# Optimization experiments

Hardware: AMD Instinct MI355X
Metric: run time of the kernel (lower is better)

The kernel has to match this reference:

```python
import jax, jax.numpy as jnp
import numpy as np

NH = 8      # nhead in TransformerEncoderLayer(cin, 8, cin, rate)
EPS = 1e-5  # torch LayerNorm default


def _ln(x, g, b):
    m = jnp.mean(x, -1, keepdims=True)
    v = jnp.mean((x - m) ** 2, -1, keepdims=True)
    return (x - m) / jnp.sqrt(v + EPS) * g + b


def _mha(q_in, kv_in, qkv_w, qkv_b, o_w, o_b):
    # q_in: (S, n, c) seq-first, kv_in: (T, n, c); torch MHA packed in_proj
    S, n, c = q_in.shape
    T = kv_in.shape[0]
    dh = c // NH
    q = q_in @ qkv_w[:c].T + qkv_b[:c]
    k = kv_in @ qkv_w[c:2 * c].T + qkv_b[c:2 * c]
    v = kv_in @ qkv_w[2 * c:].T + qkv_b[2 * c:]
    qh = q.reshape(S, n, NH, dh).transpose(1, 2, 0, 3)  # (n, NH, S, dh)
    kh = k.reshape(T, n, NH, dh).transpose(1, 2, 0, 3)
    vh = v.reshape(T, n, NH, dh).transpose(1, 2, 0, 3)
    attn = jax.nn.softmax(jnp.einsum('bhsd,bhtd->bhst', qh, kh) / np.sqrt(dh).astype(np.float32), -1)
    o = jnp.einsum('bhst,bhtd->bhsd', attn, vh).transpose(2, 0, 1, 3).reshape(S, n, c)
    return o @ o_w.T + o_b


def _enc(x, p):
    # torch post-norm encoder layer, relu activation, dropout off (eval)
    (qkv_w, qkv_b, o_w, o_b, ln1w, ln1b, ln2w, ln2b, f1w, f1b, f2w, f2b) = p
    for i in range(qkv_w.shape[0]):
        x = _ln(x + _mha(x, x, qkv_w[i], qkv_b[i], o_w[i], o_b[i]), ln1w[i], ln1b[i])
        h = jax.nn.relu(x @ f1w[i].T + f1b[i]) @ f2w[i].T + f2b[i]
        x = _ln(x + h, ln2w[i], ln2b[i])
    return x


def _dec(x, mem, p):
    (sqkv_w, sqkv_b, so_w, so_b, cqkv_w, cqkv_b, co_w, co_b,
     ln1w, ln1b, ln2w, ln2b, ln3w, ln3b, f1w, f1b, f2w, f2b) = p
    for i in range(sqkv_w.shape[0]):
        x = _ln(x + _mha(x, x, sqkv_w[i], sqkv_b[i], so_w[i], so_b[i]), ln1w[i], ln1b[i])
        x = _ln(x + _mha(x, mem, cqkv_w[i], cqkv_b[i], co_w[i], co_b[i]), ln2w[i], ln2b[i])
        h = jax.nn.relu(x @ f1w[i].T + f1b[i]) @ f2w[i].T + f2b[i]
        x = _ln(x + h, ln3w[i], ln3b[i])
    return x


def _pe2d(c, h, w):
    # standard 2D sinusoidal PE: half channels encode w, half encode h
    half = c // 2
    div = jnp.exp(jnp.arange(0, half, 2, dtype=jnp.float32) * (-np.log(10000.0) / half))
    ph = jnp.arange(h, dtype=jnp.float32)[:, None] * div
    pw = jnp.arange(w, dtype=jnp.float32)[:, None] * div
    pe_h = jnp.stack([jnp.sin(ph), jnp.cos(ph)], -1).reshape(h, half)
    pe_w = jnp.stack([jnp.sin(pw), jnp.cos(pw)], -1).reshape(w, half)
    return jnp.concatenate([
        jnp.broadcast_to(pe_w[None], (h, w, half)),
        jnp.broadcast_to(pe_h[:, None], (h, w, half)),
    ], -1)  # (h, w, c)


def setup_inputs() -> dict:
    key = jax.random.key(0)
    N, C, H, W, K, L = 8, 512, 32, 32, 4096, 6
    ks = iter(jax.random.split(key, 64))
    p = lambda *s: jax.random.normal(next(ks), s, jnp.float32) * 0.02
    return dict(
        x=jax.random.normal(next(ks), (N, C, H, W), jnp.float32),
        pre_w=p(C, C), pre_b=p(C), post_w=p(C, C), post_b=p(C),
        cb_w=p(C, K),  # codebook.weight: (cin, k)
        e_qkv_w=p(L, 3 * C, C), e_qkv_b=p(L, 3 * C), e_o_w=p(L, C, C), e_o_b=p(L, C),
        e_ln1_w=jnp.ones((L, C)), e_ln1_b=jnp.zeros((L, C)),
        e_ln2_w=jnp.ones((L, C)), e_ln2_b=jnp.zeros((L, C)),
        e_f1_w=p(L, C, C), e_f1_b=p(L, C), e_f2_w=p(L, C, C), e_f2_b=p(L, C),
        d_sqkv_w=p(L, 3 * C, C), d_sqkv_b=p(L, 3 * C), d_so_w=p(L, C, C), d_so_b=p(L, C),
        d_cqkv_w=p(L, 3 * C, C), d_cqkv_b=p(L, 3 * C), d_co_w=p(L, C, C), d_co_b=p(L, C),
        d_ln1_w=jnp.ones((L, C)), d_ln1_b=jnp.zeros((L, C)),
        d_ln2_w=jnp.ones((L, C)), d_ln2_b=jnp.zeros((L, C)),
        d_ln3_w=jnp.ones((L, C)), d_ln3_b=jnp.zeros((L, C)),
        d_f1_w=p(L, C, C), d_f1_b=p(L, C), d_f2_w=p(L, C, C), d_f2_b=p(L, C),
        mask=jax.random.bernoulli(next(ks), 0.5, (H * W, N, 1)),  # mixin=1.0 -> p=0.5
    )


def reference(x, pre_w, pre_b, post_w, post_b, cb_w,
              e_qkv_w, e_qkv_b, e_o_w, e_o_b, e_ln1_w, e_ln1_b, e_ln2_w, e_ln2_b,
              e_f1_w, e_f1_b, e_f2_w, e_f2_b,
              d_sqkv_w, d_sqkv_b, d_so_w, d_so_b, d_cqkv_w, d_cqkv_b, d_co_w, d_co_b,
              d_ln1_w, d_ln1_b, d_ln2_w, d_ln2_b, d_ln3_w, d_ln3_b,
              d_f1_w, d_f1_b, d_f2_w, d_f2_b, mask):
    n, c, h, w = x.shape
    S = h * w
    enc_in = jnp.transpose(x, (2, 3, 0, 1))  # (h, w, n, c)
    posisted = (enc_in + _pe2d(c, h, w)[:, :, None, :]).reshape(S, n, c)
    enc_flat = enc_in.reshape(S, n, c)
    y = _enc(posisted, (e_qkv_w, e_qkv_b, e_o_w, e_o_b, e_ln1_w, e_ln1_b,
                        e_ln2_w, e_ln2_b, e_f1_w, e_f1_b, e_f2_w, e_f2_b))
    pre = y @ pre_w.T + pre_b                        # (S, n, c) preProcess
    high = jnp.transpose(pre, (1, 2, 0)).reshape(n, c, h, w)
    sim = jnp.einsum('snc,ck->snk', pre, cb_w)       # similarity (S, n, K)
    logits = jnp.transpose(sim, (1, 0, 2)).reshape(n, h, w, -1)
    soft = jax.nn.softmax(sim, -1) @ cb_w.T          # codebook(softmax) (S, n, c)
    code = jnp.argmax(sim, -1)                        # (S, n)
    hard = cb_w.T[code]                               # one_hot @ cb_w.T == gather
    quant = jax.lax.stop_gradient(hard - soft) + soft  # straight-through
    softs = jnp.transpose(soft, (1, 2, 0)).reshape(n, c, h, w)
    hards = jnp.transpose(hard, (1, 2, 0)).reshape(n, c, h, w)
    post = quant @ post_w.T + post_b                  # postProcess
    mixed = jnp.where(mask, jax.lax.stop_gradient(enc_flat), post)
    dec = _dec(mixed, post, (d_sqkv_w, d_sqkv_b, d_so_w, d_so_b, d_cqkv_w, d_cqkv_b,
                             d_co_w, d_co_b, d_ln1_w, d_ln1_b, d_ln2_w, d_ln2_b,
                             d_ln3_w, d_ln3_b, d_f1_w, d_f1_b, d_f2_w, d_f2_b))
    quantized = jnp.transpose(dec, (1, 2, 0)).reshape(n, c, h, w)
    codes = jnp.transpose(code, (1, 0)).reshape(n, h, w)
    return (quantized, high, softs, hards, codes, logits)
```

## Files before the change

kernel.cpp:

```cpp
#include <hip/hip_runtime.h>
#include <math.h>

#define S_LEN 1024
#define NB 8
#define CDIM 512
#define KCB 4096
#define DH 64
#define NLAYER 6
#define NTOK (S_LEN*NB)
#define TOKC ((long)NTOK*CDIM)

typedef __attribute__((ext_vector_type(8))) _Float16 f16x8;
typedef __attribute__((ext_vector_type(4))) _Float16 f16x4;
typedef __attribute__((ext_vector_type(2))) _Float16 f16x2;
typedef __attribute__((ext_vector_type(4))) float f32x4;

template<int TM, int SPLIT, int F16IN, bool BIAS, bool RES, bool RELU, bool OREMAP, bool E16>
__global__ __launch_bounds__(256)
void hgemm_k(const void* __restrict__ Av, const void* __restrict__ Wv,
             const float* __restrict__ bias, const float* __restrict__ Rsrc, int ldr,
             float* __restrict__ C, int ldc, int M, int N, int K,
             _Float16* __restrict__ Ch16, _Float16* __restrict__ Cl16,
             const void* __restrict__ Avl, const void* __restrict__ Wvl)
{
  constexpr int MI = TM / 32;
  constexpr int ATPR = 256 / TM;
  constexpr int ACOL = 64 / ATPR;
  constexpr bool AF16 = (F16IN >= 1);
  constexpr bool WF16 = (F16IN == 1 || F16IN == 2);
  __shared__ __align__(16) _Float16 Ah[TM*64];
  __shared__ __align__(16) _Float16 Bh[128*64];
  __shared__ __align__(16) _Float16 Al[SPLIT ? TM*64 : 8];
  __shared__ __align__(16) _Float16 Bl[SPLIT ? 128*64 : 8];
  const int t = threadIdx.x;
  const int m0 = blockIdx.y * TM, n0 = blockIdx.x * 128;

  const int arow = t / ATPR, apart = t % ATPR;
  const int brow = t >> 1, bpart = t & 1;

  const float*    Af  = (const float*)Av;
  const _Float16* Axh = (const _Float16*)Av;
  const _Float16* Axl = (const _Float16*)Avl;
  const float*    Wf  = (const float*)Wv;
  const _Float16* Wxh = (const _Float16*)Wv;
  const _Float16* Wxl = (const _Float16*)Wvl;
  const long aoff = (long)(m0 + arow) * K + apart * ACOL;
  const long boff = (long)(n0 + brow) * K + bpart * 32;

  const int lane = t & 63, wave = t >> 6;
  const int wm = wave >> 1, wn = wave & 1;
  const int lr = lane & 15, lk = lane >> 4;

  f32x4 acc[MI][4];
#pragma unroll
  for (int mi = 0; mi < MI; ++mi)
#pragma unroll
    for (int ni = 0; ni < 4; ++ni)
#pragma unroll
      for (int e = 0; e < 4; ++e) acc[mi][ni][e] = 0.f;

  float4 a4[ACOL/4], b4[8];
  f16x8  a16[ACOL/8], b16[4];
  f16x8  a16l[F16IN==2 ? ACOL/8 : 1], b16l[F16IN==2 ? 4 : 1];
  if (AF16) {
#pragma unroll
    for (int g = 0; g < ACOL/8; ++g) a16[g] = *(const f16x8*)(Axh + aoff + g*8);
    if (F16IN == 2) {
#pragma unroll
      for (int g = 0; g < ACOL/8; ++g) a16l[g] = *(const f16x8*)(Axl + aoff + g*8);
    }
  } else {
#pragma unroll
    for (int j = 0; j < ACOL/4; ++j) a4[j] = *(const float4*)(Af + aoff + j*4);
  }
  if (WF16) {
#pragma unroll
    for (int g = 0; g < 4; ++g) b16[g] = *(const f16x8*)(Wxh + boff + g*8);
    if (F16IN == 2) {
#pragma unroll
      for (int g = 0; g < 4; ++g) b16l[g] = *(const f16x8*)(Wxl + boff + g*8);
    }
  } else {
#pragma unroll
    for (int j = 0; j < 8; ++j) b4[j] = *(const float4*)(Wf + boff + j*4);
  }

  for (int k0 = 0; k0 < K; k0 += 64) {
    __syncthreads();
    if (AF16) {
#pragma unroll
      for (int g = 0; g < ACOL/8; ++g) {
        const int sw = (apart*ACOL*2 + g*16) ^ ((arow & 7) << 4);
        *(f16x8*)((char*)Ah + arow*128 + sw) = a16[g];
        if (F16IN == 2) *(f16x8*)((char*)Al + arow*128 + sw) = a16l[g];
      }
    } else {
      const float* af = (const float*)a4;
#pragma unroll
      for (int g = 0; g < ACOL/8; ++g) {
        f16x8 h, l;
#pragma unroll
        for (int j = 0; j < 8; ++j) {
          float xv = af[g*8+j];
          _Float16 hh = (_Float16)xv;
          h[j] = hh;
          if (SPLIT) l[j] = (_Float16)(xv - (float)hh);
        }
        const int sw = (apart*ACOL*2 + g*16) ^ ((arow & 7) << 4);
        *(f16x8*)((char*)Ah + arow*128 + sw) = h;
        if (SPLIT) *(f16x8*)((char*)Al + arow*128 + sw) = l;
      }
    }
    if (WF16) {
#pragma unroll
      for (int g = 0; g < 4; ++g) {
        const int sw = (bpart*64 + g*16) ^ ((brow & 7) << 4);
        *(f16x8*)((char*)Bh + brow*128 + sw) = b16[g];
        if (F16IN == 2) *(f16x8*)((char*)Bl + brow*128 + sw) = b16l[g];
      }
    } else {
      const float* bf = (const float*)b4;
#pragma unroll
      for (int g = 0; g < 4; ++g) {
        f16x8 h, l;
#pragma unroll
        for (int j = 0; j < 8; ++j) {
          float xv = bf[g*8+j];
          _Float16 hh = (_Float16)xv;
          h[j] = hh;
          if (SPLIT) l[j] = (_Float16)(xv - (float)hh);
        }
        const int sw = (bpart*64 + g*16) ^ ((brow & 7) << 4);
        *(f16x8*)((char*)Bh + brow*128 + sw) = h;
        if (SPLIT) *(f16x8*)((char*)Bl + brow*128 + sw) = l;
      }
    }
    __syncthreads();
    if (k0 + 64 < K) {
      if (AF16) {
#pragma unroll
        for (int g = 0; g < ACOL/8; ++g) a16[g] = *(const f16x8*)(Axh + aoff + k0 + 64 + g*8);
        if (F16IN == 2) {
#pragma unroll
          for (int g = 0; g < ACOL/8; ++g) a16l[g] = *(const f16x8*)(Axl + aoff + k0 + 64 + g*8);
        }
      } else {
#pragma unroll
        for (int j = 0; j < ACOL/4; ++j) a4[j] = *(const float4*)(Af + aoff + k0 + 64 + j*4);
      }
      if (WF16) {
#pragma unroll
        for (int g = 0; g < 4; ++g) b16[g] = *(const f16x8*)(Wxh + boff + k0 + 64 + g*8);
        if (F16IN == 2) {
#pragma unroll
          for (int g = 0; g < 4; ++g) b16l[g] = *(const f16x8*)(Wxl + boff + k0 + 64 + g*8);
        }
      } else {
#pragma unroll
        for (int j = 0; j < 8; ++j) b4[j] = *(const float4*)(Wf + boff + k0 + 64 + j*4);
      }
    }
#pragma unroll
    for (int kk = 0; kk < 2; ++kk) {
      f16x8 afh[MI], bfh[4], afl[MI], bfl[4];
#pragma unroll
      for (int mi = 0; mi < MI; ++mi) {
        const int r = wm*(TM/2) + mi*16 + lr;
        const int bo = (lk*16 + kk*64) ^ ((r & 7) << 4);
        afh[mi] = *(const f16x8*)((const char*)Ah + r*128 + bo);
        if (SPLIT) afl[mi] = *(const f16x8*)((const char*)Al + r*128 + bo);
      }
#pragma unroll
      for (int ni = 0; ni < 4; ++ni) {
        const int r = wn*64 + ni*16 + lr;
        const int bo = (lk*16 + kk*64) ^ ((r & 7) << 4);
        bfh[ni] = *(const f16x8*)((const char*)Bh + r*128 + bo);
        if (SPLIT) bfl[ni] = *(const f16x8*)((const char*)Bl + r*128 + bo);
      }
#pragma unroll
      for (int mi = 0; mi < MI; ++mi)
#pragma unroll
        for (int ni = 0; ni < 4; ++ni) {
          acc[mi][ni] = __builtin_amdgcn_mfma_f32_16x16x32_f16(afh[mi], bfh[ni], acc[mi][ni], 0, 0, 0);
          if (SPLIT) {
            acc[mi][ni] = __builtin_amdgcn_mfma_f32_16x16x32_f16(afh[mi], bfl[ni], acc[mi][ni], 0, 0, 0);
            acc[mi][ni] = __builtin_amdgcn_mfma_f32_16x16x32_f16(afl[mi], bfh[ni], acc[mi][ni], 0, 0, 0);
          }
        }
    }
  }

  float bvv[4];
  if (BIAS) {
#pragma unroll
    for (int ni = 0; ni < 4; ++ni) bvv[ni] = bias[n0 + wn*64 + ni*16 + lr];
  }
#pragma unroll
  for (int mi = 0; mi < MI; ++mi)
#pragma unroll
  for (int i = 0; i < 4; ++i) {
    const int rm = m0 + wm*(TM/2) + mi*16 + lk*4 + i;
    long orow = rm;
    if (OREMAP) orow = (long)(rm & (NB-1)) * S_LEN + (rm >> 3);
#pragma unroll
    for (int ni = 0; ni < 4; ++ni) {
      const int col = n0 + wn*64 + ni*16 + lr;
      float v = acc[mi][ni][i];
      if (BIAS) v += bvv[ni];
      if (RES)  v += Rsrc[(long)rm*ldr + col];
      if (RELU) v = fmaxf(v, 0.f);
      if (E16) {
        _Float16 hv = (_Float16)v;
        Ch16[(long)rm*ldc + col] = hv;
        if (SPLIT) Cl16[(long)rm*ldc + col] = (_Float16)(v - (float)hv);
        if (C != nullptr) C[orow*(long)ldc + col] = v;
      } else {
        C[orow*(long)ldc + col] = v;
      }
    }
  }
}

template<int SPLIT>
__global__ __launch_bounds__(256)
void sattn_k(const _Float16* __restrict__ Qh, const _Float16* __restrict__ Ql, int ldq,
             const _Float16* __restrict__ Kh, const _Float16* __restrict__ Kl, int ldk,
             const _Float16* __restrict__ Vh, const _Float16* __restrict__ Vl, int ldv,
             _Float16* __restrict__ Oh, _Float16* __restrict__ Ol, int ldo)
{
  __shared__ __align__(16) char Kb[8192];
  __shared__ __align__(16) char Vb[8192];
  __shared__ __align__(16) char Klo[SPLIT ? 8192 : 16];
  __shared__ __align__(16) char Vlo[SPLIT ? 8192 : 16];

  const int t = threadIdx.x;
  const int b = blockIdx.x >> 3, hd = blockIdx.x & 7;
  const int s0 = blockIdx.y * 128;
  const int qoff = hd * DH;
  const int wave = t >> 6, lane = t & 63;
  const int lr = lane & 15, lk = lane >> 4;
  const int krow = t >> 2, kqd = t & 3;
  const int vtp = t & 31, vdc = t >> 5;

  f16x8 qa[2][2], qal[2][2];
#pragma unroll
  for (int qb = 0; qb < 2; ++qb)
#pragma unroll
    for (int kk = 0; kk < 2; ++kk) {
      const int q = s0 + wave*32 + qb*16 + lr;
      const long base = ((long)q*NB + b)*ldq + qoff + kk*32 + lk*8;
      f16x8 v = *(const f16x8*)(Qh + base);
#pragma unroll
      for (int e = 0; e < 8; ++e) v[e] = v[e] * (_Float16)0.125f;
      qa[qb][kk] = v;
      if (SPLIT) {
        f16x8 w = *(const f16x8*)(Ql + base);
#pragma unroll
        for (int e = 0; e < 8; ++e) w[e] = w[e] * (_Float16)0.125f;
        qal[qb][kk] = w;
      }
    }

  float m_run[2] = {-INFINITY, -INFINITY};
  float l_run[2] = {0.f, 0.f};
  f32x4 oaccT[4][2];
#pragma unroll
  for (int nd = 0; nd < 4; ++nd)
#pragma unroll
    for (int qb = 0; qb < 2; ++qb)
#pragma unroll
      for (int e = 0; e < 4; ++e) oaccT[nd][qb][e] = 0.f;

  f16x8 kr0, kr1, krl0, krl1, vr0, vr1, vrl0, vrl1;
  {
    const long kb = ((long)krow*NB + b)*ldk + qoff + kqd*16;
    kr0 = *(const f16x8*)(Kh + kb);
    kr1 = *(const f16x8*)(Kh + kb + 8);
    if (SPLIT) { krl0 = *(const f16x8*)(Kl + kb); krl1 = *(const f16x8*)(Kl + kb + 8); }
    const long vb = ((long)(2*vtp)*NB + b)*ldv + qoff + vdc*8;
    vr0 = *(const f16x8*)(Vh + vb);
    vr1 = *(const f16x8*)(Vh + vb + (long)NB*ldv);
    if (SPLIT) { vrl0 = *(const f16x8*)(Vl + vb); vrl1 = *(const f16x8*)(Vl + vb + (long)NB*ldv); }
  }

  for (int t0 = 0; t0 < S_LEN; t0 += 64) {
    __syncthreads();
    {
      const int sw0 = (kqd*32) ^ ((krow & 7) << 4);
      const int sw1 = (kqd*32 + 16) ^ ((krow & 7) << 4);
      *(f16x8*)(Kb + krow*128 + sw0) = kr0;
      *(f16x8*)(Kb + krow*128 + sw1) = kr1;
      if (SPLIT) {
        *(f16x8*)(Klo + krow*128 + sw0) = krl0;
        *(f16x8*)(Klo + krow*128 + sw1) = krl1;
      }
#pragma unroll
      for (int j = 0; j < 8; ++j) {
        const int dd = vdc*8 + j;
        const int off = dd*128 + ((vtp*4) ^ ((dd & 7) << 4));
        f16x2 hv = {vr0[j], vr1[j]};
        *(f16x2*)(Vb + off) = hv;
        if (SPLIT) {
          f16x2 lv = {vrl0[j], vrl1[j]};
          *(f16x2*)(Vlo + off) = lv;
        }
      }
    }
    if (t0 + 64 < S_LEN) {
      const long kb = ((long)(t0 + 64 + krow)*NB + b)*ldk + qoff + kqd*16;
      kr0 = *(const f16x8*)(Kh + kb);
      kr1 = *(const f16x8*)(Kh + kb + 8);
      if (SPLIT) { krl0 = *(const f16x8*)(Kl + kb); krl1 = *(const f16x8*)(Kl + kb + 8); }
      const long vb = ((long)(t0 + 64 + 2*vtp)*NB + b)*ldv + qoff + vdc*8;
      vr0 = *(const f16x8*)(Vh + vb);
      vr1 = *(const f16x8*)(Vh + vb + (long)NB*ldv);
      if (SPLIT) { vrl0 = *(const f16x8*)(Vl + vb); vrl1 = *(const f16x8*)(Vl + vb + (long)NB*ldv); }
    }
    __syncthreads();

    f32x4 st[4][2];
#pragma unroll
    for (int ki = 0; ki < 4; ++ki)
#pragma unroll
      for (int qb = 0; qb < 2; ++qb)
#pragma unroll
        for (int e = 0; e < 4; ++e) st[ki][qb][e] = 0.f;
#pragma unroll
    for (int kk = 0; kk < 2; ++kk) {
      f16x8 kb[4], kbl[4];
#pragma unroll
      for (int ki = 0; ki < 4; ++ki) {
        const int r = ki*16 + lr;
        const int bo = (lk*16 + kk*64) ^ ((r & 7) << 4);
        kb[ki] = *(const f16x8*)(Kb + r*128 + bo);
        if (SPLIT) kbl[ki] = *(const f16x8*)(Klo + r*128 + bo);
      }
#pragma unroll
      for (int ki = 0; ki < 4; ++ki)
#pragma unroll
        for (int qb = 0; qb < 2; ++qb) {
          st[ki][qb] = __builtin_amdgcn_mfma_f32_16x16x32_f16(kb[ki], qa[qb][kk], st[ki][qb], 0, 0, 0);
          if (SPLIT) {
            st[ki][qb] = __builtin_amdgcn_mfma_f32_16x16x32_f16(kb[ki], qal[qb][kk], st[ki][qb], 0, 0, 0);
            st[ki][qb] = __builtin_amdgcn_mfma_f32_16x16x32_f16(kbl[ki], qa[qb][kk], st[ki][qb], 0, 0, 0);
          }
        }
    }

    f16x4 pbh[4][2], pbl[4][2];
#pragma unroll
    for (int qb = 0; qb < 2; ++qb) {
      float rm = st[0][qb][0];
#pragma unroll
      for (int ki = 0; ki < 4; ++ki)
#pragma unroll
        for (int e = 0; e < 4; ++e) rm = fmaxf(rm, st[ki][qb][e]);
      rm = fmaxf(rm, __shfl_xor(rm, 16));
      rm = fmaxf(rm, __shfl_xor(rm, 32));
      const float mnew = fmaxf(m_run[qb], rm);
      const float corr = __expf(m_run[qb] - mnew);
      m_run[qb] = mnew;
      float ls = 0.f;
#pragma unroll
      for (int ki = 0; ki < 4; ++ki) {
        f16x4 ph, pl;
#pragma unroll
        for (int e = 0; e < 4; ++e) {
          float p = __expf(st[ki][qb][e] - mnew);
          ls += p;
          _Float16 h = (_Float16)p;
          ph[e] = h;
          if (SPLIT) pl[e] = (_Float16)(p - (float)h);
        }
        pbh[ki][qb] = ph;
        if (SPLIT) pbl[ki][qb] = pl;
      }
      ls += __shfl_xor(ls, 16);
      ls += __shfl_xor(ls, 32);
      l_run[qb] = l_run[qb]*corr + ls;
#pragma unroll
      for (int nd = 0; nd < 4; ++nd)
#pragma unroll
        for (int e = 0; e < 4; ++e) oaccT[nd][qb][e] *= corr;
    }

#pragma unroll
    for (int ki = 0; ki < 4; ++ki) {
      f16x4 avh[4], avl[4];
#pragma unroll
      for (int nd = 0; nd < 4; ++nd) {
        const int row = nd*16 + lr;
        const int bo = (ki*32 + lk*8) ^ ((row & 7) << 4);
        avh[nd] = *(const f16x4*)(Vb + row*128 + bo);
        if (SPLIT) avl[nd] = *(const f16x4*)(Vlo + row*128 + bo);
      }
#pragma unroll
      for (int nd = 0; nd < 4; ++nd)
#pragma unroll
        for (int qb = 0; qb < 2; ++qb) {
          oaccT[nd][qb] = __builtin_amdgcn_mfma_f32_16x16x16f16(avh[nd], pbh[ki][qb], oaccT[nd][qb], 0, 0, 0);
          if (SPLIT) {
            oaccT[nd][qb] = __builtin_amdgcn_mfma_f32_16x16x16f16(avh[nd], pbl[ki][qb], oaccT[nd][qb], 0, 0, 0);
            oaccT[nd][qb] = __builtin_amdgcn_mfma_f32_16x16x16f16(avl[nd], pbh[ki][qb], oaccT[nd][qb], 0, 0, 0);
          }
        }
    }
  }

#pragma unroll
  for (int qb = 0; qb < 2; ++qb) {
    const float inv = 1.0f / l_run[qb];
    const int q = s0 + wave*32 + qb*16 + lr;
    const long base = ((long)q * NB + b) * ldo + qoff;
#pragma unroll
    for (int nd = 0; nd < 4; ++nd) {
      f16x4 o, ol;
#pragma unroll
      for (int e = 0; e < 4; ++e) {
        float v = oaccT[nd][qb][e] * inv;
        _Float16 h = (_Float16)v;
        o[e] = h;
        if (SPLIT) ol[e] = (_Float16)(v - (float)h);
      }
      *(f16x4*)(Oh + base + nd*16 + lk*4) = o;
      if (SPLIT) *(f16x4*)(Ol + base + nd*16 + lk*4) = ol;
    }
  }
}

template<int ES>
__global__ __launch_bounds__(256)
void ln_k(const float* __restrict__ X, const float* __restrict__ g,
          const float* __restrict__ bb, float* __restrict__ Y,
          _Float16* __restrict__ Yh, _Float16* __restrict__ Yl)
{
  const int t = threadIdx.x;
  const int lane = t & 63;
  const long row = (long)blockIdx.x * 4 + (t >> 6);
  const float* xr = X + row * CDIM;
  float4 v0 = *(const float4*)(xr + lane*4);
  float4 v1 = *(const float4*)(xr + 256 + lane*4);
  float s = v0.x+v0.y+v0.z+v0.w + v1.x+v1.y+v1.z+v1.w;
#pragma unroll
  for (int off = 1; off < 64; off <<= 1) s += __shfl_xor(s, off);
  const float mean = s * (1.0f/512.0f);
  float d[8] = {v0.x-mean, v0.y-mean, v0.z-mean, v0.w-mean,
                v1.x-mean, v1.y-mean, v1.z-mean, v1.w-mean};
  float sq = d[0]*d[0]+d[1]*d[1]+d[2]*d[2]+d[3]*d[3]
           + d[4]*d[4]+d[5]*d[5]+d[6]*d[6]+d[7]*d[7];
#pragma unroll
  for (int off = 1; off < 64; off <<= 1) sq += __shfl_xor(sq, off);
  const float inv = 1.0f / sqrtf(sq * (1.0f/512.0f) + 1e-5f);
  float4 g0 = *(const float4*)(g + lane*4);
  float4 g1 = *(const float4*)(g + 256 + lane*4);
  float4 b0 = *(const float4*)(bb + lane*4);
  float4 b1 = *(const float4*)(bb + 256 + lane*4);
  float o[8];
  o[0] = d[0]*inv*g0.x + b0.x; o[1] = d[1]*inv*g0.y + b0.y;
  o[2] = d[2]*inv*g0.z + b0.z; o[3] = d[3]*inv*g0.w + b0.w;
  o[4] = d[4]*inv*g1.x + b1.x; o[5] = d[5]*inv*g1.y + b1.y;
  o[6] = d[6]*inv*g1.z + b1.z; o[7] = d[7]*inv*g1.w + b1.w;
  *(float4*)(Y + row*CDIM + lane*4) = *(float4*)&o[0];
  *(float4*)(Y + row*CDIM + 256 + lane*4) = *(float4*)&o[4];
  if (ES) {
    f16x4 h0, h1, l0, l1;
#pragma unroll
    for (int j = 0; j < 4; ++j) {
      _Float16 h = (_Float16)o[j];     h0[j] = h;
      _Float16 k = (_Float16)o[4+j];   h1[j] = k;
      if (ES == 1) { l0[j] = (_Float16)(o[j] - (float)h); l1[j] = (_Float16)(o[4+j] - (float)k); }
    }
    *(f16x4*)(Yh + row*CDIM + lane*4) = h0;
    *(f16x4*)(Yh + row*CDIM + 256 + lane*4) = h1;
    if (ES == 1) {
      *(f16x4*)(Yl + row*CDIM + lane*4) = l0;
      *(f16x4*)(Yl + row*CDIM + 256 + lane*4) = l1;
    }
  }
}

__global__ void pack_pe_k(const float* __restrict__ x, float* __restrict__ encf,
                          float* __restrict__ posd,
                          _Float16* __restrict__ posh, _Float16* __restrict__ posl)
{
  __shared__ float tl[32][33];
  const int b = blockIdx.z;
  const int s0 = blockIdx.x*32, c0 = blockIdx.y*32;
#pragma unroll
  for (int i = 0; i < 4; ++i) {
    int ci = threadIdx.y + i*8;
    tl[ci][threadIdx.x] = x[((long)b*CDIM + c0+ci)*S_LEN + s0 + threadIdx.x];
  }
  __syncthreads();
#pragma unroll
  for (int i = 0; i < 4; ++i) {
    int si = threadIdx.y + i*8;
    int s = s0 + si;
    int ch = c0 + threadIdx.x;
    float val = tl[threadIdx.x][si];
    long o = ((long)s*NB + b)*CDIM + ch;
    encf[o] = val;
    int pos = (ch < 256) ? (s & 31) : (s >> 5);
    int j = (ch & 255) >> 1;
    float dv = expf((float)(2*j) * (-9.210340371976184f / 256.0f));
    float ang = (float)pos * dv;
    float pe = (ch & 1) ? cosf(ang) : sinf(ang);
    float pv = val + pe;
    posd[o] = pv;
    _Float16 h = (_Float16)pv;
    posh[o] = h;
    posl[o] = (_Float16)(pv - (float)h);
  }
}

__global__ void tpose_k(const float* __restrict__ in, float* __restrict__ out)
{
  __shared__ float tl[32][33];
  const int b = blockIdx.z;
  const int s0 = blockIdx.x*32, c0 = blockIdx.y*32;
#pragma unroll
  for (int i = 0; i < 4; ++i) {
    int si = threadIdx.y + i*8;
    tl[si][threadIdx.x] = in[((long)(s0+si)*NB + b)*CDIM + c0 + threadIdx.x];
  }
  __syncthreads();
#pragma unroll
  for (int i = 0; i < 4; ++i) {
    int ci = threadIdx.y + i*8;
    out[((long)b*CDIM + c0+ci)*S_LEN + s0 + threadIdx.x] = tl[threadIdx.x][ci];
  }
}

__global__ void cbt16_k(const float* __restrict__ cb,
                        _Float16* __restrict__ outh, _Float16* __restrict__ outl)
{
  __shared__ float tl[32][33];
  const int k0 = blockIdx.x*32, c0 = blockIdx.y*32;
#pragma unroll
  for (int i = 0; i < 4; ++i) {
    int ci = threadIdx.y + i*8;
    tl[ci][threadIdx.x] = cb[(long)(c0+ci)*KCB + k0 + threadIdx.x];
  }
  __syncthreads();
#pragma unroll
  for (int i = 0; i < 4; ++i) {
    int ki = threadIdx.y + i*8;
    float v = tl[threadIdx.x][ki];
    _Float16 h = (_Float16)v;
    outh[(long)(k0+ki)*CDIM + c0 + threadIdx.x] = h;
    outl[(long)(k0+ki)*CDIM + c0 + threadIdx.x] = (_Float16)(v - (float)h);
  }
}

__global__ __launch_bounds__(256)
void conv16_k(const float* __restrict__ in, _Float16* __restrict__ out)
{
  const long i = ((long)blockIdx.x * 256 + threadIdx.x) * 8;
  float4 v0 = *(const float4*)(in + i);
  float4 v1 = *(const float4*)(in + i + 4);
  f16x8 h;
  h[0]=(_Float16)v0.x; h[1]=(_Float16)v0.y; h[2]=(_Float16)v0.z; h[3]=(_Float16)v0.w;
  h[4]=(_Float16)v1.x; h[5]=(_Float16)v1.y; h[6]=(_Float16)v1.z; h[7]=(_Float16)v1.w;
  *(f16x8*)(out + i) = h;
}

__global__ __launch_bounds__(256)
void convsplit_k(const float* __restrict__ in, _Float16* __restrict__ oh,
                 _Float16* __restrict__ ol)
{
  const long i = ((long)blockIdx.x * 256 + threadIdx.x) * 8;
  float4 v0 = *(const float4*)(in + i);
  float4 v1 = *(const float4*)(in + i + 4);
  float vv[8] = {v0.x,v0.y,v0.z,v0.w,v1.x,v1.y,v1.z,v1.w};
  f16x8 h, l;
#pragma unroll
  for (int j = 0; j < 8; ++j) {
    _Float16 hh = (_Float16)vv[j];
    h[j] = hh;
    l[j] = (_Float16)(vv[j] - (float)hh);
  }
  *(f16x8*)(oh + i) = h;
  *(f16x8*)(ol + i) = l;
}

__global__ __launch_bounds__(256)
void simstats_k(const float* __restrict__ logits, _Float16* __restrict__ Pbuf,
                int* __restrict__ codes_tok, float* __restrict__ codes_out)
{
  const long phys = blockIdx.x;
  const float* rowp = logits + phys * KCB;
  const int t = threadIdx.x;
  float vals[16];
#pragma unroll
  for (int rep = 0; rep < 4; ++rep) {
    float4 v = *(const float4*)(rowp + rep*1024 + t*4);
    vals[rep*4+0]=v.x; vals[rep*4+1]=v.y; vals[rep*4+2]=v.z; vals[rep*4+3]=v.w;
  }
  float mv = -INFINITY; int mi = 0;
#pragma unroll
  for (int rep = 0; rep < 4; ++rep)
#pragma unroll
    for (int j = 0; j < 4; ++j) {
      float xv = vals[rep*4+j];
      int ix = rep*1024 + t*4 + j;
      if (xv > mv) { mv = xv; mi = ix; }
    }
  const int lane = t & 63, wid = t >> 6;
#pragma unroll
  for (int off = 1; off < 64; off <<= 1) {
    float ov = __shfl_xor(mv, off);
    int   oi = __shfl_xor(mi, off);
    if (ov > mv || (ov == mv && oi < mi)) { mv = ov; mi = oi; }
  }
  __shared__ float smax[4]; __shared__ int sidx[4]; __shared__ float ssum[4];
  __shared__ float fm; __shared__ int fi; __shared__ float sinv;
  if (lane == 0) { smax[wid] = mv; sidx[wid] = mi; }
  __syncthreads();
  if (t == 0) {
    float bm = smax[0]; int bi = sidx[0];
    for (int wq = 1; wq < 4; ++wq)
      if (smax[wq] > bm || (smax[wq] == bm && sidx[wq] < bi)) { bm = smax[wq]; bi = sidx[wq]; }
    fm = bm; fi = bi;
  }
  __syncthreads();
  const float Mx = fm;
  float se = 0.f;
#pragma unroll
  for (int q = 0; q < 16; ++q) se += __expf(vals[q] - Mx);
#pragma unroll
  for (int off = 1; off < 64; off <<= 1) se += __shfl_xor(se, off);
  if (lane == 0) ssum[wid] = se;
  __syncthreads();
  const int b = (int)(phys >> 10), s = (int)(phys & 1023);
  if (t == 0) {
    float tot = ssum[0]+ssum[1]+ssum[2]+ssum[3];
    sinv = 1.0f / tot;
    codes_tok[s*NB + b] = fi;
    codes_out[phys] = (float)fi;
  }
  __syncthreads();
  const float inv = sinv;
  _Float16* prow = Pbuf + ((long)s*NB + b) * KCB;
#pragma unroll
  for (int rep = 0; rep < 4; ++rep) {
    f16x4 pv;
#pragma unroll
    for (int j = 0; j < 4; ++j) pv[j] = (_Float16)(__expf(vals[rep*4+j] - Mx) * inv);
    *(f16x4*)(prow + rep*1024 + t*4) = pv;
  }
}

__global__ __launch_bounds__(128)
void quant_k(const float* __restrict__ soft, const int* __restrict__ codes_tok,
             const _Float16* __restrict__ cbh, const _Float16* __restrict__ cbl,
             float* __restrict__ quant, float* __restrict__ hardb,
             _Float16* __restrict__ qh16)
{
  const int r = blockIdx.x;
  const int code = codes_tok[r];
  const int c = threadIdx.x * 4;
  f16x4 hh = *(const f16x4*)(cbh + (long)code*CDIM + c);
  f16x4 hl = *(const f16x4*)(cbl + (long)code*CDIM + c);
  float4 sf = *(const float4*)(soft + (long)r*CDIM + c);
  float4 h, q;
  h.x = (float)hh[0] + (float)hl[0]; h.y = (float)hh[1] + (float)hl[1];
  h.z = (float)hh[2] + (float)hl[2]; h.w = (float)hh[3] + (float)hl[3];
  q.x = (h.x - sf.x) + sf.x; q.y = (h.y - sf.y) + sf.y;
  q.z = (h.z - sf.z) + sf.z; q.w = (h.w - sf.w) + sf.w;
  *(float4*)(quant + (long)r*CDIM + c) = q;
  *(float4*)(hardb + (long)r*CDIM + c) = h;
  f16x4 qh = {(_Float16)q.x, (_Float16)q.y, (_Float16)q.z, (_Float16)q.w};
  *(f16x4*)(qh16 + (long)r*CDIM + c) = qh;
}

__global__ void maskdetect_k(const void* __restrict__ mask, int* __restrict__ flag)
{
  const unsigned int* wds = (const unsigned int*)mask;
  int t = threadIdx.x;
  int okI = 1, okF = 1, okL = 1;
  for (int i = t; i < 2048; i += 256) {
    unsigned int u = wds[i];
    if (u > 1u) okI = 0;
    if (u != 0u && u != 0x3F800000u) okF = 0;
    if ((i & 1) ? (u != 0u) : (u > 1u)) okL = 0;
  }
  __shared__ int sI, sF, sL;
  if (t == 0) { sI = 1; sF = 1; sL = 1; }
  __syncthreads();
  if (!okI) atomicAnd(&sI, 0);
  if (!okF) atomicAnd(&sF, 0);
  if (!okL) atomicAnd(&sL, 0);
  __syncthreads();
  if (t == 0) {
    int f;
    if (sI && sL) f = 3;
    else if (sI)  f = 1;
    else if (sF)  f = 2;
    else          f = 0;
    *flag = f;
  }
}

__global__ __launch_bounds__(256)
void mixed_k(const float* __restrict__ encf, const float* __restrict__ post,
             const void* __restrict__ mask, const int* __restrict__ flag,
             float* __restrict__ outx, _Float16* __restrict__ outh)
{
  long gid = (long)blockIdx.x * blockDim.x + threadIdx.x;
  int r = (int)(gid >> 7);
  int c = (int)(gid & 127) * 4;
  int f = *flag;
  bool mv;
  if (f == 0)      mv = ((const unsigned char*)mask)[r] != 0;
  else if (f == 1) mv = ((const int*)mask)[r] != 0;
  else if (f == 3) mv = ((const long long*)mask)[r] != 0;
  else             mv = ((const float*)mask)[r] != 0.0f;
  const float* src = mv ? encf : post;
  float4 v = *(const float4*)(src + (long)r*CDIM + c);
  *(float4*)(outx + (long)r*CDIM + c) = v;
  f16x4 h = {(_Float16)v.x, (_Float16)v.y, (_Float16)v.z, (_Float16)v.w};
  *(f16x4*)(outh + (long)r*CDIM + c) = h;
}

extern "C" void kernel_launch(void* const* d_in, const int* in_sizes, int n_in,
                              void* d_out, int out_size, void* d_ws, size_t ws_size,
                              hipStream_t stream)
{
  const float* x       = (const float*)d_in[0];
  const float* pre_w   = (const float*)d_in[1];
  const float* pre_b   = (const float*)d_in[2];
  const float* post_w  = (const float*)d_in[3];
  const float* post_b  = (const float*)d_in[4];
  const float* cb_w    = (const float*)d_in[5];
  const float* e_qkv_w = (const float*)d_in[6];
  const float* e_qkv_b = (const float*)d_in[7];
  const float* e_o_w   = (const float*)d_in[8];
  const float* e_o_b   = (const float*)d_in[9];
  const float* e_ln1_w = (const float*)d_in[10];
  const float* e_ln1_b = (const float*)d_in[11];
  const float* e_ln2_w = (const float*)d_in[12];
  const float* e_ln2_b = (const float*)d_in[13];
  const float* e_f1_w  = (const float*)d_in[14];
  const float* e_f1_b  = (const float*)d_in[15];
  const float* e_f2_w  = (const float*)d_in[16];
  const float* e_f2_b  = (const float*)d_in[17];
  const float* d_sqkv_w= (const float*)d_in[18];
  const float* d_sqkv_b= (const float*)d_in[19];
  const float* d_so_w  = (const float*)d_in[20];
  const float* d_so_b  = (const float*)d_in[21];
  const float* d_cqkv_w= (const float*)d_in[22];
  const float* d_cqkv_b= (const float*)d_in[23];
  const float* d_co_w  = (const float*)d_in[24];
  const float* d_co_b  = (const float*)d_in[25];
  const float* d_ln1w  = (const float*)d_in[26];
  const float* d_ln1b  = (const float*)d_in[27];
  const float* d_ln2w  = (const float*)d_in[28];
  const float* d_ln2b  = (const float*)d_in[29];
  const float* d_ln3w  = (const float*)d_in[30];
  const float* d_ln3b  = (const float*)d_in[31];
  const float* d_f1w   = (const float*)d_in[32];
  const float* d_f1b   = (const float*)d_in[33];
  const float* d_f2w   = (const float*)d_in[34];
  const float* d_f2b   = (const float*)d_in[35];
  const void*  mask    = d_in[36];

  float* out = (float*)d_out;
  float* o_quant  = out;
  float* o_high   = out + 4194304;
  float* o_softs  = out + 8388608;
  float* o_hards  = out + 12582912;
  float* o_codes  = out + 16777216;
  float* o_logits = out + 16785408;

  float* ws    = (float*)d_ws;
  float* ENC   = ws;
  float* Xb    = ws + TOKC;
  float* T1    = ws + 2*TOKC;
  float* T2    = ws + 3*TOKC;
  float* QKV   = ws + 4*TOKC;
  float* MEMB  = ws + 7*TOKC;
  float* CBREG = ws + 8*TOKC;
  int*   CODES = (int*)(CBREG + (long)KCB*CDIM);
  int*   FLAG  = CODES + NTOK;
  float* HARDB = QKV;
  float* QUANT = QKV + TOKC;
  _Float16* PBUF = (_Float16*)QKV;
  _Float16* CBH  = (_Float16*)T1;
  _Float16* QKVh = (_Float16*)QKV;
  _Float16* QKVl = QKVh + (long)NTOK*3*CDIM;
  _Float16* CQh  = (_Float16*)QKV;
  _Float16* KVh  = (_Float16*)(QKV + TOKC);
  _Float16* CBT16h = (_Float16*)CBREG;
  _Float16* CBT16l = CBT16h + (long)KCB*CDIM;
  _Float16* PREH = (_Float16*)T2;
  _Float16* PREL = PREH + TOKC;
  _Float16* AH16   = (_Float16*)ENC;
  _Float16* FH16   = AH16 + TOKC;
  _Float16* XH16   = ((_Float16*)QKV) + 4*TOKC;
  _Float16* MEMBH16= XH16 + TOKC;
  _Float16* QH16   = ((_Float16*)T1) + TOKC;

  const long WQSZ = (long)6*3*CDIM*CDIM;
  const long WSSZ = (long)6*CDIM*CDIM;
  _Float16* SCR  = (_Float16*)o_logits;
  _Float16* WQH = SCR;            _Float16* WQL = WQH + WQSZ;
  _Float16* WOH = WQL + WQSZ;     _Float16* WOL = WOH + WSSZ;
  _Float16* WF1H= WOL + WSSZ;     _Float16* WF1L= WF1H + WSSZ;
  _Float16* WF2H= WF1L + WSSZ;    _Float16* WF2L= WF2H + WSSZ;
  _Float16* WPH = WF2L + WSSZ;    _Float16* WPL = WPH + (long)CDIM*CDIM;
  _Float16* XH  = WPL + (long)CDIM*CDIM;  _Float16* XL  = XH + TOKC;
  _Float16* AH  = XL + TOKC;      _Float16* AL  = AH + TOKC;
  _Float16* L1H = AL + TOKC;      _Float16* L1L = L1H + TOKC;
  _Float16* H1H = L1L + TOKC;     _Float16* H1L = H1H + TOKC;

  _Float16* DWSQ = (_Float16*)MEMB;
  _Float16* DWCQ = (_Float16*)T1;
  _Float16* DWF1 = DWCQ + WQSZ;
  _Float16* DWF2 = DWF1 + WSSZ;
  _Float16* DWSO = (_Float16*)CBREG;
  _Float16* DWCO = DWSO + WSSZ;

  const size_t NEED = (size_t)(8*TOKC + (long)KCB*CDIM + 2*NTOK + NTOK + 16) * 4;
  if (ws_size < NEED) return;

  const int M = NTOK;
  dim3 tgrid(S_LEN/32, CDIM/32, NB), tblk(32, 8);
  dim3 agrid(NB*8, S_LEN/128);

  pack_pe_k<<<tgrid, tblk, 0, stream>>>(x, ENC, Xb, XH, XL);
  cbt16_k<<<dim3(KCB/32, CDIM/32), tblk, 0, stream>>>(cb_w, CBT16h, CBT16l);
  maskdetect_k<<<1, 256, 0, stream>>>(mask, FLAG);
  convsplit_k<<<(int)(WQSZ/2048), 256, 0, stream>>>(e_qkv_w, WQH, WQL);
  convsplit_k<<<(int)(WSSZ/2048), 256, 0, stream>>>(e_o_w,  WOH,  WOL);
  convsplit_k<<<(int)(WSSZ/2048), 256, 0, stream>>>(e_f1_w, WF1H, WF1L);
  convsplit_k<<<(int)(WSSZ/2048), 256, 0, stream>>>(e_f2_w, WF2H, WF2L);
  convsplit_k<<<(int)(((long)CDIM*CDIM)/2048), 256, 0, stream>>>(pre_w, WPH, WPL);

  for (int i = 0; i < NLAYER; ++i) {
    hgemm_k<128,1,2,true,false,false,false,true><<<dim3(3*CDIM/128, M/128), 256, 0, stream>>>(
        XH, WQH + (long)i*3*CDIM*CDIM, e_qkv_b + i*3*CDIM, nullptr, 0,
        nullptr, 3*CDIM, M, 3*CDIM, CDIM, QKVh, QKVl, XL, WQL + (long)i*3*CDIM*CDIM);
    sattn_k<1><<<agrid, 256, 0, stream>>>(QKVh, QKVl, 3*CDIM,
        QKVh+CDIM, QKVl+CDIM, 3*CDIM, QKVh+2*CDIM, QKVl+2*CDIM, 3*CDIM,
        AH, AL, CDIM);
    hgemm_k<64,1,2,true,true,false,false,false><<<dim3(CDIM/128, M/64), 256, 0, stream>>>(
        AH, WOH + (long)i*CDIM*CDIM, e_o_b + i*CDIM, Xb, CDIM,
        T2, CDIM, M, CDIM, CDIM, nullptr, nullptr, AL, WOL + (long)i*CDIM*CDIM);
    ln_k<1><<<M/4, 256, 0, stream>>>(T2, e_ln1_w + i*CDIM, e_ln1_b + i*CDIM, T1, L1H, L1L);
    hgemm_k<64,1,2,true,false,true,false,true><<<dim3(CDIM/128, M/64), 256, 0, stream>>>(
        L1H, WF1H + (long)i*CDIM*CDIM, e_f1_b + i*CDIM, nullptr, 0,
        nullptr, CDIM, M, CDIM, CDIM, H1H, H1L, L1L, WF1L + (long)i*CDIM*CDIM);
    hgemm_k<64,1,2,true,true,false,false,false><<<dim3(CDIM/128, M/64), 256, 0, stream>>>(
        H1H, WF2H + (long)i*CDIM*CDIM, e_f2_b + i*CDIM, T1, CDIM,
        T2, CDIM, M, CDIM, CDIM, nullptr, nullptr, H1L, WF2L + (long)i*CDIM*CDIM);
    ln_k<1><<<M/4, 256, 0, stream>>>(T2, e_ln2_w + i*CDIM, e_ln2_b + i*CDIM, Xb, XH, XL);
  }

  hgemm_k<64,1,2,true,false,false,false,true><<<dim3(CDIM/128, M/64), 256, 0, stream>>>(
      XH, WPH, pre_b, nullptr, 0, T1, CDIM, M, CDIM, CDIM, PREH, PREL, XL, WPL);
  tpose_k<<<tgrid, tblk, 0, stream>>>(T1, o_high);
  hgemm_k<128,1,2,false,false,false,true,false><<<dim3(KCB/128, M/128), 256, 0, stream>>>(
      PREH, CBT16h, nullptr, nullptr, 0, o_logits, KCB, M, KCB, CDIM,
      nullptr, nullptr, PREL, CBT16l);
  conv16_k<<<(CDIM*(long)KCB)/(256*8), 256, 0, stream>>>(cb_w, CBH);
  simstats_k<<<NTOK, 256, 0, stream>>>(o_logits, PBUF, CODES, o_codes);
  hgemm_k<64,0,1,false,false,false,false,false><<<dim3(CDIM/128, M/64), 256, 0, stream>>>(
      PBUF, CBH, nullptr, nullptr, 0, T2, CDIM, M, CDIM, KCB,
      nullptr, nullptr, nullptr, nullptr);
  tpose_k<<<tgrid, tblk, 0, stream>>>(T2, o_softs);
  quant_k<<<NTOK, 128, 0, stream>>>(T2, CODES, CBT16h, CBT16l, QUANT, HARDB, QH16);
  tpose_k<<<tgrid, tblk, 0, stream>>>(HARDB, o_hards);
  conv16_k<<<(int)(WSSZ/2048), 256, 0, stream>>>(d_so_w, DWSO);
  conv16_k<<<(int)(WSSZ/2048), 256, 0, stream>>>(d_co_w, DWCO);
  hgemm_k<64,0,3,true,false,false,false,true><<<dim3(CDIM/128, M/64), 256, 0, stream>>>(
      QH16, post_w, post_b, nullptr, 0, MEMB, CDIM, M, CDIM, CDIM,
      MEMBH16, nullptr, nullptr, nullptr);
  conv16_k<<<(int)(WQSZ/2048), 256, 0, stream>>>(d_cqkv_w, DWCQ);
  conv16_k<<<(int)(WSSZ/2048), 256, 0, stream>>>(d_f1w, DWF1);
  conv16_k<<<(int)(WSSZ/2048), 256, 0, stream>>>(d_f2w, DWF2);
  mixed_k<<<4096, 256, 0, stream>>>(ENC, MEMB, mask, FLAG, Xb, XH16);
  conv16_k<<<(int)(WQSZ/2048), 256, 0, stream>>>(d_sqkv_w, DWSQ);

  for (int i = 0; i < NLAYER; ++i) {
    hgemm_k<128,0,1,true,false,false,false,true><<<dim3(3*CDIM/128, M/128), 256, 0, stream>>>(
        XH16, DWSQ + (long)i*3*CDIM*CDIM, d_sqkv_b + i*3*CDIM, nullptr, 0,
        nullptr, 3*CDIM, M, 3*CDIM, CDIM, QKVh, nullptr, nullptr, nullptr);
    sattn_k<0><<<agrid, 256, 0, stream>>>(QKVh, nullptr, 3*CDIM,
        QKVh+CDIM, nullptr, 3*CDIM, QKVh+2*CDIM, nullptr, 3*CDIM,
        AH16, nullptr, CDIM);
    hgemm_k<64,0,1,true,true,false,false,false><<<dim3(CDIM/128, M/64), 256, 0, stream>>>(
        AH16, DWSO + (long)i*CDIM*CDIM, d_so_b + i*CDIM, Xb, CDIM,
        T2, CDIM, M, CDIM, CDIM, nullptr, nullptr, nullptr, nullptr);
    ln_k<2><<<M/4, 256, 0, stream>>>(T2, d_ln1w + i*CDIM, d_ln1b + i*CDIM, Xb, XH16, nullptr);
    hgemm_k<64,0,1,true,false,false,false,true><<<dim3(CDIM/128, M/64), 256, 0, stream>>>(
        XH16, DWCQ + (long)i*3*CDIM*CDIM, d_cqkv_b + i*3*CDIM, nullptr, 0,
        nullptr, CDIM, M, CDIM, CDIM, CQh, nullptr, nullptr, nullptr);
    hgemm_k<128,0,1,true,false,false,false,true><<<dim3(2*CDIM/128, M/128), 256, 0, stream>>>(
        MEMBH16, DWCQ + (long)i*3*CDIM*CDIM + (long)CDIM*CDIM,
        d_cqkv_b + i*3*CDIM + CDIM, nullptr, 0,
        nullptr, 2*CDIM, M, 2*CDIM, CDIM, KVh, nullptr, nullptr, nullptr);
    sattn_k<0><<<agrid, 256, 0, stream>>>(CQh, nullptr, CDIM,
        KVh, nullptr, 2*CDIM, KVh+CDIM, nullptr, 2*CDIM,
        AH16, nullptr, CDIM);
    hgemm_k<64,0,1,true,true,false,false,false><<<dim3(CDIM/128, M/64), 256, 0, stream>>>(
        AH16, DWCO + (long)i*CDIM*CDIM, d_co_b + i*CDIM, Xb, CDIM,
        T2, CDIM, M, CDIM, CDIM, nullptr, nullptr, nullptr, nullptr);
    ln_k<2><<<M/4, 256, 0, stream>>>(T2, d_ln2w + i*CDIM, d_ln2b + i*CDIM, Xb, XH16, nullptr);
    hgemm_k<64,0,1,true,false,true,false,true><<<dim3(CDIM/128, M/64), 256, 0, stream>>>(
        XH16, DWF1 + (long)i*CDIM*CDIM, d_f1b + i*CDIM, nullptr, 0,
        nullptr, CDIM, M, CDIM, CDIM, FH16, nullptr, nullptr, nullptr);
    hgemm_k<64,0,1,true,true,false,false,false><<<dim3(CDIM/128, M/64), 256, 0, stream>>>(
        FH16, DWF2 + (long)i*CDIM*CDIM, d_f2b + i*CDIM, Xb, CDIM,
        T2, CDIM, M, CDIM, CDIM, nullptr, nullptr, nullptr, nullptr);
    ln_k<2><<<M/4, 256, 0, stream>>>(T2, d_ln3w + i*CDIM, d_ln3b + i*CDIM, Xb, XH16, nullptr);
  }
  tpose_k<<<tgrid, tblk, 0, stream>>>(Xb, o_quant);
}
```

Before: 2.722 ms.

## Add 128-key-tile flash attention kernel with register-prefetched K/V for decoder

Adds a dedicated fp16 flash-attention kernel that processes 128 keys per tile. It uses XOR-swizzled LDS layouts for K and transposed V, and prefetches the next K/V tile into registers while the current tile is computed. Q is pre-scaled by 1/sqrt(dh) in fp16, and the kernel uses 16x16x32 MFMAs for QK^T. It replaces the generic sattn_k in both decoder self- and cross-attention, aiming to cut sync and LDS traffic per key. In exchange it uses more registers, which may lower occupancy.

```diff
diff --git a/kernel.cpp b/kernel.cpp
--- a/kernel.cpp
+++ b/kernel.cpp
@@ -424,6 +424,172 @@
       }
       *(f16x4*)(Oh + base + nd*16 + lk*4) = o;
       if (SPLIT) *(f16x4*)(Ol + base + nd*16 + lk*4) = ol;
+    }
+  }
+}
+
+__global__ __launch_bounds__(256)
+void sattn128_k(const _Float16* __restrict__ Qh, int ldq,
+                const _Float16* __restrict__ Kh, int ldk,
+                const _Float16* __restrict__ Vh, int ldv,
+                _Float16* __restrict__ Oh, int ldo)
+{
+  __shared__ __align__(16) char Kb[16384];
+  __shared__ __align__(16) char Vb[16384];
+
+  const int t = threadIdx.x;
+  const int b = blockIdx.x >> 3, hd = blockIdx.x & 7;
+  const int s0 = blockIdx.y * 128;
+  const int qoff = hd * DH;
+  const int wave = t >> 6, lane = t & 63;
+  const int lr = lane & 15, lk = lane >> 4;
+  const int krow = t >> 1, kpart = t & 1;
+  const int vtp = t & 63, vdc = t >> 6;
+
+  f16x8 qa[2][2];
+#pragma unroll
+  for (int qb = 0; qb < 2; ++qb)
+#pragma unroll
+    for (int kk = 0; kk < 2; ++kk) {
+      const int q = s0 + wave*32 + qb*16 + lr;
+      const long base = ((long)q*NB + b)*ldq + qoff + kk*32 + lk*8;
+      f16x8 v = *(const f16x8*)(Qh + base);
+#pragma unroll
+      for (int e = 0; e < 8; ++e) v[e] = v[e] * (_Float16)0.125f;
+      qa[qb][kk] = v;
+    }
+
+  float m_run[2] = {-INFINITY, -INFINITY};
+  float l_run[2] = {0.f, 0.f};
+  f32x4 oaccT[4][2];
+#pragma unroll
+  for (int nd = 0; nd < 4; ++nd)
+#pragma unroll
+    for (int qb = 0; qb < 2; ++qb)
+#pragma unroll
+      for (int e = 0; e < 4; ++e) oaccT[nd][qb][e] = 0.f;
+
+  f16x8 kr[4], vrA[2], vrB[2];
+  {
+    const long kb = ((long)krow*NB + b)*ldk + qoff + kpart*32;
+#pragma unroll
+    for (int g = 0; g < 4; ++g) kr[g] = *(const f16x8*)(Kh + kb + g*8);
+    const long vb = ((long)(2*vtp)*NB + b)*ldv + qoff + vdc*16;
+    vrA[0] = *(const f16x8*)(Vh + vb);
+    vrA[1] = *(const f16x8*)(Vh + vb + 8);
+    vrB[0] = *(const f16x8*)(Vh + vb + (long)NB*ldv);
+    vrB[1] = *(const f16x8*)(Vh + vb + (long)NB*ldv + 8);
+  }
+
+  for (int t0 = 0; t0 < S_LEN; t0 += 128) {
+    __syncthreads();
+    {
+#pragma unroll
+      for (int g = 0; g < 4; ++g) {
+        const int sw = (kpart*64 + g*16) ^ ((krow & 7) << 4);
+        *(f16x8*)(Kb + krow*128 + sw) = kr[g];
+      }
+#pragma unroll
+      for (int h = 0; h < 2; ++h)
+#pragma unroll
+        for (int j = 0; j < 8; ++j) {
+          const int dd = vdc*16 + h*8 + j;
+          const int off = dd*256 + ((vtp*4) ^ ((dd & 7) << 4));
+          f16x2 hv = {vrA[h][j], vrB[h][j]};
+          *(f16x2*)(Vb + off) = hv;
+        }
+    }
+    if (t0 + 128 < S_LEN) {
+      const long kb = ((long)(t0 + 128 + krow)*NB + b)*ldk + qoff + kpart*32;
+#pragma unroll
+      for (int g = 0; g < 4; ++g) kr[g] = *(const f16x8*)(Kh + kb + g*8);
+      const long vb = ((long)(t0 + 128 + 2*vtp)*NB + b)*ldv + qoff + vdc*16;
+      vrA[0] = *(const f16x8*)(Vh + vb);
+      vrA[1] = *(const f16x8*)(Vh + vb + 8);
+      vrB[0] = *(const f16x8*)(Vh + vb + (long)NB*ldv);
+      vrB[1] = *(const f16x8*)(Vh + vb + (long)NB*ldv + 8);
+    }
+    __syncthreads();
+
+    f32x4 st[8][2];
+#pragma unroll
+    for (int ki = 0; ki < 8; ++ki)
+#pragma unroll
+      for (int qb = 0; qb < 2; ++qb)
+#pragma unroll
+        for (int e = 0; e < 4; ++e) st[ki][qb][e] = 0.f;
+#pragma unroll
+    for (int kk = 0; kk < 2; ++kk) {
+#pragma unroll
+      for (int ki = 0; ki < 8; ++ki) {
+        const int r = ki*16 + lr;
+        const int bo = (lk*16 + kk*64) ^ ((r & 7) << 4);
+        f16x8 kbv = *(const f16x8*)(Kb + r*128 + bo);
+#pragma unroll
+        for (int qb = 0; qb < 2; ++qb)
+          st[ki][qb] = __builtin_amdgcn_mfma_f32_16x16x32_f16(kbv, qa[qb][kk], st[ki][qb], 0, 0, 0);
+      }
+    }
+
+    f16x4 pbh[8][2];
+#pragma unroll
+    for (int qb = 0; qb < 2; ++qb) {
+      float rm = st[0][qb][0];
+#pragma unroll
+      for (int ki = 0; ki < 8; ++ki)
+#pragma unroll
+        for (int e = 0; e < 4; ++e) rm = fmaxf(rm, st[ki][qb][e]);
+      rm = fmaxf(rm, __shfl_xor(rm, 16));
+      rm = fmaxf(rm, __shfl_xor(rm, 32));
+      const float mnew = fmaxf(m_run[qb], rm);
+      const float corr = __expf(m_run[qb] - mnew);
+      m_run[qb] = mnew;
+      float ls = 0.f;
+#pragma unroll
+      for (int ki = 0; ki < 8; ++ki) {
+        f16x4 ph;
+#pragma unroll
+        for (int e = 0; e < 4; ++e) {
+          float p = __expf(st[ki][qb][e] - mnew);
+          ls += p;
+          ph[e] = (_Float16)p;
+        }
+        pbh[ki][qb] = ph;
+      }
+      ls += __shfl_xor(ls, 16);
+      ls += __shfl_xor(ls, 32);
+      l_run[qb] = l_run[qb]*corr + ls;
+#pragma unroll
+      for (int nd = 0; nd < 4; ++nd)
+#pragma unroll
+        for (int e = 0; e < 4; ++e) oaccT[nd][qb][e] *= corr;
+    }
+
+#pragma unroll
+    for (int ki = 0; ki < 8; ++ki) {
+#pragma unroll
+      for (int nd = 0; nd < 4; ++nd) {
+        const int row = nd*16 + lr;
+        const int bo = (ki*32 + lk*8) ^ ((row & 7) << 4);
+        f16x4 av = *(const f16x4*)(Vb + row*256 + bo);
+#pragma unroll
+        for (int qb = 0; qb < 2; ++qb)
+          oaccT[nd][qb] = __builtin_amdgcn_mfma_f32_16x16x16f16(av, pbh[ki][qb], oaccT[nd][qb], 0, 0, 0);
+      }
+    }
+  }
+
+#pragma unroll
+  for (int qb = 0; qb < 2; ++qb) {
+    const float inv = 1.0f / l_run[qb];
+    const int q = s0 + wave*32 + qb*16 + lr;
+    const long base = ((long)q * NB + b) * ldo + qoff;
+#pragma unroll
+    for (int nd = 0; nd < 4; ++nd) {
+      f16x4 o;
+#pragma unroll
+      for (int e = 0; e < 4; ++e) o[e] = (_Float16)(oaccT[nd][qb][e] * inv);
+      *(f16x4*)(Oh + base + nd*16 + lk*4) = o;
     }
   }
 }
@@ -885,9 +1051,8 @@
     hgemm_k<128,0,1,true,false,false,false,true><<<dim3(3*CDIM/128, M/128), 256, 0, stream>>>(
         XH16, DWSQ + (long)i*3*CDIM*CDIM, d_sqkv_b + i*3*CDIM, nullptr, 0,
         nullptr, 3*CDIM, M, 3*CDIM, CDIM, QKVh, nullptr, nullptr, nullptr);
-    sattn_k<0><<<agrid, 256, 0, stream>>>(QKVh, nullptr, 3*CDIM,
-        QKVh+CDIM, nullptr, 3*CDIM, QKVh+2*CDIM, nullptr, 3*CDIM,
-        AH16, nullptr, CDIM);
+    sattn128_k<<<agrid, 256, 0, stream>>>(QKVh, 3*CDIM,
+        QKVh+CDIM, 3*CDIM, QKVh+2*CDIM, 3*CDIM, AH16, CDIM);
     hgemm_k<64,0,1,true,true,false,false,false><<<dim3(CDIM/128, M/64), 256, 0, stream>>>(
         AH16, DWSO + (long)i*CDIM*CDIM, d_so_b + i*CDIM, Xb, CDIM,
         T2, CDIM, M, CDIM, CDIM, nullptr, nullptr, nullptr, nullptr);
@@ -899,9 +1064,8 @@
         MEMBH16, DWCQ + (long)i*3*CDIM*CDIM + (long)CDIM*CDIM,
         d_cqkv_b + i*3*CDIM + CDIM, nullptr, 0,
         nullptr, 2*CDIM, M, 2*CDIM, CDIM, KVh, nullptr, nullptr, nullptr);
-    sattn_k<0><<<agrid, 256, 0, stream>>>(CQh, nullptr, CDIM,
-        KVh, nullptr, 2*CDIM, KVh+CDIM, nullptr, 2*CDIM,
-        AH16, nullptr, CDIM);
+    sattn128_k<<<agrid, 256, 0, stream>>>(CQh, CDIM,
+        KVh, 2*CDIM, KVh+CDIM, 2*CDIM, AH16, CDIM);
     hgemm_k<64,0,1,true,true,false,false,false><<<dim3(CDIM/128, M/64), 256, 0, stream>>>(
         AH16, DWCO + (long)i*CDIM*CDIM, d_co_b + i*CDIM, Xb, CDIM,
         T2, CDIM, M, CDIM, CDIM, nullptr, nullptr, nullptr, nullptr);
```

Measured after the change: 2.704 ms. Within noise of the previous version (-0.6%).
